# Optimization experiments

Hardware: AMD Instinct MI355X
Metric: run time of the kernel (lower is better)

Reference implementation:

```python
import jax, jax.numpy as jnp
import numpy as np

B, T, D, H = 1, 2048, 1024, 16
DH = D // H
DFF = 4 * D
SPARSITY_LAMBDA = 0.0005
LN_EPS = 1e-5


def _ln(x, g, b):
    mu = jnp.mean(x, axis=-1, keepdims=True)
    var = jnp.mean((x - mu) ** 2, axis=-1, keepdims=True)
    return (x - mu) * jax.lax.rsqrt(var + LN_EPS) * g + b


def setup_inputs() -> dict:
    key = jax.random.key(0)
    ks = jax.random.split(key, 8)
    s = lambda fan: 1.0 / np.sqrt(fan)
    inp = {
        "x": jax.random.normal(ks[0], (B, T, D), jnp.float32),
        "causal_mask": jnp.triu(jnp.ones((T, T), jnp.bool_), 1),
        "W_qkv": jax.random.normal(ks[1], (3 * D, D), jnp.float32) * s(D),
        "W_out": jax.random.normal(ks[2], (D, D), jnp.float32) * s(D),
        "log_mask": jnp.zeros((1, H, T, T), jnp.float32),
        "W_gate": jax.random.normal(ks[3], (D, 2 * D), jnp.float32) * s(2 * D),
        "b_gate": jnp.zeros((D,), jnp.float32),
        "g1": jnp.ones((D,), jnp.float32),
        "b1": jnp.zeros((D,), jnp.float32),
        "g2": jnp.ones((D,), jnp.float32),
        "b2": jnp.zeros((D,), jnp.float32),
        "W_ff1": jax.random.normal(ks[4], (DFF, D), jnp.float32) * s(D),
        "b_ff1": jnp.zeros((DFF,), jnp.float32),
        "W_ff2": jax.random.normal(ks[5], (D, DFF), jnp.float32) * s(DFF),
        "b_ff2": jnp.zeros((D,), jnp.float32),
    }
    return inp


def reference(x, causal_mask, W_qkv, W_out, log_mask, W_gate, b_gate,
              g1, b1, g2, b2, W_ff1, b_ff1, W_ff2, b_ff2):
    Bx, Tx, Dx = x.shape
    xn = _ln(x, g1, b1)
    qkv = xn @ W_qkv.T                              # [B,T,3D]
    q, k, v = jnp.split(qkv, 3, axis=-1)
    rs = lambda t: t.reshape(Bx, Tx, H, DH).transpose(0, 2, 1, 3)  # [B,H,T,dh]
    q, k, v = rs(q), rs(k), rs(v)
    scale = jnp.sqrt(jnp.asarray(DH, x.dtype))
    qk = jnp.einsum("bhtd,bhsd->bhts", q, k) / scale  # [B,H,T,T]
    cm = causal_mask[:Tx, :Tx]
    neg = jnp.asarray(-jnp.inf, x.dtype)
    # stream 1: plain causal softmax
    a_txt = jax.nn.softmax(jnp.where(cm, neg, qk), axis=-1)
    out_txt = jnp.einsum("bhts,bhsd->bhtd", a_txt, v)
    # stream 2: sigmoid-gated scores then causal softmax
    M = jax.nn.sigmoid(log_mask[:, :, :Tx, :Tx])
    a_cau = jax.nn.softmax(jnp.where(cm, neg, qk * M), axis=-1)
    out_cau = jnp.einsum("bhts,bhsd->bhtd", a_cau, v)
    merge = lambda t: t.transpose(0, 2, 1, 3).reshape(Bx, Tx, Dx)
    cat = jnp.concatenate([merge(out_txt), merge(out_cau)], axis=-1)  # [B,T,2D]
    a = (cat @ W_gate.T + b_gate) @ W_out.T
    sp = SPARSITY_LAMBDA * jnp.mean(M)
    # residual + FFN (dropout=0, eval mode)
    h = x + a
    hn = _ln(h, g2, b2)
    ff = jax.nn.gelu(hn @ W_ff1.T + b_ff1, approximate=False) @ W_ff2.T + b_ff2
    return h + ff, sp
```

## Files before the change

### kernel.cpp

```cpp
#include <hip/hip_runtime.h>
#include <hip/hip_bf16.h>

typedef __bf16 bf16x8 __attribute__((ext_vector_type(8)));
typedef _Float16 f16x4 __attribute__((ext_vector_type(4)));
typedef float f32x4 __attribute__((ext_vector_type(4)));

#define MFMA16(a, b, c) __builtin_amdgcn_mfma_f32_16x16x32_bf16(a, b, c, 0, 0, 0)
#define MFMA16H(a, b, c) __builtin_amdgcn_mfma_f32_16x16x16f16(a, b, c, 0, 0, 0)

#define T_SEQ 2048
#define D_MODEL 1024
#define N_HEADS 16
#define HEAD_DIM 64
#define D_FF 4096
#define QKV_STRIDE 3072

__device__ __forceinline__ float sigm(float x) { return 1.f / (1.f + __expf(-x)); }

__device__ __forceinline__ void g2l16(const void* g, void* l)
{
    __builtin_amdgcn_global_load_lds(
        (const __attribute__((address_space(1))) void*)g,
        (__attribute__((address_space(3))) void*)l, 16, 0, 0);
}

__device__ __forceinline__ float bperm(int srclane, float v)
{
    return __builtin_bit_cast(float,
        __builtin_amdgcn_ds_bpermute(srclane * 4, __builtin_bit_cast(int, v)));
}

#define N8_QKV 393216
#define N8_OUT 131072
#define N8_GATE 262144
#define N8_FF1 524288
#define N8_FF2 524288
__global__ __launch_bounds__(256) void cast_all_kernel(
    const float* __restrict__ s0, const float* __restrict__ s1,
    const float* __restrict__ s2, const float* __restrict__ s3,
    const float* __restrict__ s4,
    __bf16* __restrict__ d0, __bf16* __restrict__ d1, __bf16* __restrict__ d2,
    __bf16* __restrict__ d3, __bf16* __restrict__ d4, float* __restrict__ acc)
{
    int i = blockIdx.x * 256 + threadIdx.x;
    if (i == 0) acc[0] = 0.f;
    const float* s; __bf16* d; int j;
    if (i < N8_QKV)                           { s = s0; d = d0; j = i; }
    else if (i < N8_QKV + N8_OUT)             { s = s1; d = d1; j = i - N8_QKV; }
    else if (i < N8_QKV + N8_OUT + N8_GATE)   { s = s2; d = d2; j = i - N8_QKV - N8_OUT; }
    else if (i < N8_QKV + N8_OUT + N8_GATE + N8_FF1)
        { s = s3; d = d3; j = i - N8_QKV - N8_OUT - N8_GATE; }
    else { s = s4; d = d4; j = i - N8_QKV - N8_OUT - N8_GATE - N8_FF1; }
    const float4* p = (const float4*)s + (size_t)j * 2;
    float4 a = p[0], b = p[1];
    union { __bf16 h[8]; float4 v; } u;
    u.h[0] = (__bf16)a.x; u.h[1] = (__bf16)a.y; u.h[2] = (__bf16)a.z; u.h[3] = (__bf16)a.w;
    u.h[4] = (__bf16)b.x; u.h[5] = (__bf16)b.y; u.h[6] = (__bf16)b.z; u.h[7] = (__bf16)b.w;
    ((float4*)d)[j] = u.v;
}

__global__ __launch_bounds__(256) void ln_kernel(
    const float* __restrict__ x, const float* __restrict__ g,
    const float* __restrict__ b, __bf16* __restrict__ out)
{
    const int t = blockIdx.x;
    const int tid = threadIdx.x;
    float4 xv = *(const float4*)&x[t * D_MODEL + tid * 4];
    float s = xv.x + xv.y + xv.z + xv.w;
    float ss = xv.x * xv.x + xv.y * xv.y + xv.z * xv.z + xv.w * xv.w;
    for (int off = 1; off < 64; off <<= 1) {
        s += __shfl_xor(s, off);
        ss += __shfl_xor(ss, off);
    }
    __shared__ float sb[8];
    int w = tid >> 6, lane = tid & 63;
    if (lane == 0) { sb[w] = s; sb[4 + w] = ss; }
    __syncthreads();
    s = sb[0] + sb[1] + sb[2] + sb[3];
    ss = sb[4] + sb[5] + sb[6] + sb[7];
    float mu = s * (1.f / D_MODEL);
    float var = ss * (1.f / D_MODEL) - mu * mu;
    float rs = rsqrtf(var + 1e-5f);
    const float* xp = (const float*)&xv;
    for (int i = 0; i < 4; ++i) {
        int d = tid * 4 + i;
        out[t * D_MODEL + d] = (__bf16)((xp[i] - mu) * rs * g[d] + b[d]);
    }
}

template<int BM, int EPI>
__global__ __launch_bounds__(256) void gemm_nt(
    const __bf16* __restrict__ A, const __bf16* __restrict__ B,
    const float* __restrict__ bias,
    __bf16* __restrict__ outb, float* __restrict__ outf, _Float16* __restrict__ vtout,
    int M, int N, int klen, int lda)
{
    constexpr int BN = 128;
    constexpr int STAGE = (BM + BN) * 64 * 2;
    constexpr int CTB = (EPI == 3) ? BM * BN * 4 : (EPI == 4) ? BM * 132 * 4 : BM * BN * 2;
    constexpr int SMEM = (STAGE > CTB) ? STAGE : CTB;
    __shared__ __align__(16) char smem[SMEM];
    __bf16* As = (__bf16*)smem;
    __bf16* Bs = As + BM * 64;

    const int tid = threadIdx.x;
    const int lane = tid & 63, w = tid >> 6;
    const int quad = lane >> 4, l16 = lane & 15;
    const int bm = blockIdx.x * BM, bn = blockIdx.y * BN;
    const int koff = blockIdx.z * klen;
    if (EPI == 3) outf += (size_t)blockIdx.z * M * N;
    constexpr int NI = 4;
    constexpr int NJ = (BM == 128) ? 4 : 2;
    const int wm = (BM == 128) ? (w & 1) * 64 : 0;
    const int wn = (BM == 128) ? (w >> 1) * 64 : w * 32;

    f32x4 acc[NI][NJ] = {};

    for (int k0 = 0; k0 < klen; k0 += 64) {
        __syncthreads();
        constexpr int AIT = BM * 8 / 256;
        for (int it = 0; it < AIT; ++it) {
            int c = it * 256 + tid;
            int tile = (c >= BM * 4) ? 1 : 0;
            int c2 = c & (BM * 4 - 1);
            g2l16(&A[(size_t)(bm + (c2 >> 2)) * lda + koff + k0 + tile * 32 + ((c2 & 3) << 3)],
                  &As[c * 8]);
        }
        for (int it = 0; it < 4; ++it) {
            int c = it * 256 + tid;
            int tile = (c >= 512) ? 1 : 0;
            int c2 = c & 511;
            g2l16(&B[(size_t)(bn + (c2 >> 2)) * lda + koff + k0 + tile * 32 + ((c2 & 3) << 3)],
                  &Bs[c * 8]);
        }
        __syncthreads();
        for (int ks = 0; ks < 2; ++ks) {
            bf16x8 af[NI], bfr[NJ];
            for (int i = 0; i < NI; ++i)
                af[i] = *(const bf16x8*)&As[ks * BM * 32 + (wm + i * 16 + l16) * 32 + quad * 8];
            for (int j = 0; j < NJ; ++j)
                bfr[j] = *(const bf16x8*)&Bs[ks * BN * 32 + (wn + j * 16 + l16) * 32 + quad * 8];
            for (int i = 0; i < NI; ++i)
                for (int j = 0; j < NJ; ++j)
                    acc[i][j] = MFMA16(af[i], bfr[j], acc[i][j]);
        }
    }

    __syncthreads();
    if (EPI == 3) {
        float* Ct = (float*)smem;
        for (int i = 0; i < NI; ++i)
            for (int j = 0; j < NJ; ++j)
                for (int r = 0; r < 4; ++r)
                    Ct[(wm + i * 16 + quad * 4 + r) * BN + wn + j * 16 + l16] = acc[i][j][r];
        __syncthreads();
        constexpr int IT = BM * BN / 4 / 256;
        for (int it = 0; it < IT; ++it) {
            int c = it * 256 + tid;
            int row = c >> 5, col = (c & 31) << 2;
            *(float4*)&outf[(size_t)(bm + row) * N + bn + col] = *(float4*)&Ct[row * BN + col];
        }
    } else if (EPI == 4) {
        float* Ct = (float*)smem;
        for (int i = 0; i < NI; ++i)
            for (int j = 0; j < NJ; ++j)
                for (int r = 0; r < 4; ++r)
                    Ct[(wm + i * 16 + quad * 4 + r) * 132 + wn + j * 16 + l16] = acc[i][j][r];
        __syncthreads();
        if (bn < 2048) {
            for (int it = 0; it < BM * BN / 8 / 256; ++it) {
                int c = it * 256 + tid;
                int row = c >> 4, col8 = (c & 15) << 3;
                float4 f0 = *(float4*)&Ct[row * 132 + col8];
                float4 f1 = *(float4*)&Ct[row * 132 + col8 + 4];
                union { __bf16 h[8]; float4 v; } u;
                u.h[0] = (__bf16)f0.x; u.h[1] = (__bf16)f0.y; u.h[2] = (__bf16)f0.z; u.h[3] = (__bf16)f0.w;
                u.h[4] = (__bf16)f1.x; u.h[5] = (__bf16)f1.y; u.h[6] = (__bf16)f1.z; u.h[7] = (__bf16)f1.w;
                *(float4*)&outb[(size_t)(bm + row) * N + bn + col8] = u.v;
            }
        } else {
            int col = tid & 127;
            int r0 = (tid >> 7) * 32;
            int gcol = bn - 2048 + col;
            _Float16 buf[32];
            for (int r = 0; r < 32; ++r)
                buf[r] = (_Float16)Ct[(r0 + r) * 132 + col];
            _Float16* dst = &vtout[(size_t)gcol * T_SEQ + bm + r0];
            for (int k = 0; k < 4; ++k)
                *(float4*)&dst[k * 8] = *(float4*)&buf[k * 8];
        }
    } else {
        __bf16* Ct = (__bf16*)smem;
        for (int i = 0; i < NI; ++i)
            for (int j = 0; j < NJ; ++j)
                for (int r = 0; r < 4; ++r) {
                    int row = wm + i * 16 + quad * 4 + r;
                    int col = wn + j * 16 + l16;
                    float v = acc[i][j][r];
                    if (bias) v += bias[bn + col];
                    if (EPI == 1) v = 0.5f * v * (1.f + erff(v * 0.70710678118f));
                    Ct[row * BN + col] = (__bf16)v;
                }
        __syncthreads();
        constexpr int IT = BM * BN / 8 / 256;
        for (int it = 0; it < IT; ++it) {
            int c = it * 256 + tid;
            int row = c >> 4, col = (c & 15) << 3;
            *(float4*)&outb[(size_t)(bm + row) * N + bn + col] = *(float4*)&Ct[row * BN + col];
        }
    }
}

template<int MODE>
__global__ __launch_bounds__(256) void combine_kernel(
    const float* __restrict__ p0, const float* __restrict__ p1,
    const float* __restrict__ bias, const float* __restrict__ resid,
    __bf16* __restrict__ outb, float* __restrict__ outf,
    const float* __restrict__ sigacc)
{
    int i = blockIdx.x * 256 + threadIdx.x;
    float4 a = ((const float4*)p0)[i];
    float4 b = ((const float4*)p1)[i];
    int col = (i & 255) << 2;
    float4 bb = *(const float4*)&bias[col];
    float v[4] = {a.x + b.x + bb.x, a.y + b.y + bb.y, a.z + b.z + bb.z, a.w + b.w + bb.w};
    if (MODE == 2) {
        float4 r = ((const float4*)resid)[i];
        v[0] += r.x; v[1] += r.y; v[2] += r.z; v[3] += r.w;
        float4 o = {v[0], v[1], v[2], v[3]};
        ((float4*)outf)[i] = o;
        if (i == 0)
            outf[(size_t)T_SEQ * D_MODEL] = 0.0005f * sigacc[0] * (1.f / 67108864.f);
    } else {
        union { __bf16 h[4]; float2 f2; } u;
        for (int e = 0; e < 4; ++e) u.h[e] = (__bf16)v[e];
        ((float2*)outb)[i] = u.f2;
    }
}

__global__ __launch_bounds__(256) void combine_ln_kernel(
    const float* __restrict__ p0, const float* __restrict__ p1,
    const float* __restrict__ resid, const float* __restrict__ g,
    const float* __restrict__ b, float* __restrict__ h_out,
    __bf16* __restrict__ hn_out)
{
    const int t = blockIdx.x, tid = threadIdx.x;
    const int i = t * 256 + tid;
    float4 a = ((const float4*)p0)[i];
    float4 bb = ((const float4*)p1)[i];
    float4 r = ((const float4*)resid)[i];
    float4 v = {a.x + bb.x + r.x, a.y + bb.y + r.y, a.z + bb.z + r.z, a.w + bb.w + r.w};
    ((float4*)h_out)[i] = v;
    float s = v.x + v.y + v.z + v.w;
    float ss = v.x * v.x + v.y * v.y + v.z * v.z + v.w * v.w;
    for (int off = 1; off < 64; off <<= 1) {
        s += __shfl_xor(s, off);
        ss += __shfl_xor(ss, off);
    }
    __shared__ float sb[8];
    int w = tid >> 6, lane = tid & 63;
    if (lane == 0) { sb[w] = s; sb[4 + w] = ss; }
    __syncthreads();
    s = sb[0] + sb[1] + sb[2] + sb[3];
    ss = sb[4] + sb[5] + sb[6] + sb[7];
    float mu = s * (1.f / D_MODEL);
    float var = ss * (1.f / D_MODEL) - mu * mu;
    float rs = rsqrtf(var + 1e-5f);
    const float* vp = (const float*)&v;
    union { __bf16 h[4]; float2 f2; } u;
    for (int k = 0; k < 4; ++k) {
        int d = tid * 4 + k;
        u.h[k] = (__bf16)((vp[k] - mu) * rs * g[d] + b[d]);
    }
    ((float2*)hn_out)[i] = u.f2;
}

__global__ __launch_bounds__(256) void attn_split_kernel(
    const __bf16* __restrict__ qkv, const _Float16* __restrict__ vt,
    const float* __restrict__ lmask,
    __bf16* __restrict__ part_O, float2* __restrict__ part_ml,
    float* __restrict__ sigacc)
{
    __shared__ __bf16 KsAll[2 * 4096];
    __shared__ _Float16 VsAll[2 * 4096];

    const int tid = threadIdx.x;
    const int w = tid >> 6, lane = tid & 63;
    const int quad = lane >> 4, l16 = lane & 15;
    const int idx = blockIdx.x, h = blockIdx.y;
    int qt, sp;
    if (idx < 8)       { qt = idx;                sp = 0; }
    else if (idx < 24) { qt = 8 + ((idx - 8) >> 1);  sp = (idx - 8) & 1; }
    else if (idx < 48) { qt = 16 + (idx - 24) / 3;   sp = (idx - 24) % 3; }
    else               { qt = 24 + ((idx - 48) >> 2); sp = (idx - 48) & 3; }
    const int q0 = qt * 64;
    const int sbeg = sp * 512;
    const int send = min(sbeg + 512, q0 + 64);
    const int nch = (send - sbeg) >> 6;

    auto stage = [&](int s0, int bsel) {
        __bf16* kd = &KsAll[bsel * 4096];
        _Float16* vd = &VsAll[bsel * 4096];
        for (int it = 0; it < 2; ++it) {
            int c = it * 256 + tid;
            int tile = c >> 8, c2 = c & 255;
            g2l16(&qkv[(size_t)(s0 + (c2 >> 2)) * QKV_STRIDE + 1024 + h * 64 + tile * 32 + ((c2 & 3) << 3)],
                  &kd[c * 8]);
        }
        for (int it = 0; it < 2; ++it) {
            int c = it * 256 + tid;
            int dh = c >> 3, g = c & 7;
            int sIn = ((g + dh) & 7) * 8;
            g2l16(&vt[((size_t)h * 64 + dh) * T_SEQ + s0 + sIn], &vd[c * 8]);
        }
    };

    const int tq = q0 + w * 16 + l16;
    bf16x8 qf0 = *(const bf16x8*)&qkv[(size_t)tq * QKV_STRIDE + h * 64 + quad * 8];
    bf16x8 qf1 = *(const bf16x8*)&qkv[(size_t)tq * QKV_STRIDE + h * 64 + 32 + quad * 8];

    float m_[2] = {-1e30f, -1e30f}, l_[2] = {0.f, 0.f};
    f32x4 O[2][4] = {};
    float sigsum = 0.f;

    stage(sbeg, 0);

    for (int ci = 0; ci < nch; ++ci) {
        const int s0 = sbeg + (ci << 6);
        const int cur = ci & 1;
        __syncthreads();

        float4 lm[4];
        for (int c = 0; c < 4; ++c)
            lm[c] = *(const float4*)&lmask[((size_t)h * T_SEQ + tq) * T_SEQ + s0 + c * 16 + quad * 4];
        float4 up[4];
        const bool lower = (s0 + 64 <= q0);
        if (lower) {
            const float* upp = &lmask[((size_t)h * T_SEQ + s0 + (tid >> 2)) * T_SEQ + q0 + ((tid & 3) << 4)];
            for (int k = 0; k < 4; ++k) up[k] = *(const float4*)&upp[k * 4];
        }

        if (ci + 1 < nch) stage(s0 + 64, cur ^ 1);

        const __bf16* Ks = &KsAll[cur * 4096];
        const _Float16* Vs = &VsAll[cur * 4096];

        f32x4 St[4];
        for (int c = 0; c < 4; ++c) {
            bf16x8 kf0 = *(const bf16x8*)&Ks[(c * 16 + l16) * 32 + quad * 8];
            bf16x8 kf1 = *(const bf16x8*)&Ks[2048 + (c * 16 + l16) * 32 + quad * 8];
            f32x4 z = {};
            z = MFMA16(kf0, qf0, z);
            z = MFMA16(kf1, qf1, z);
            St[c] = z * 0.125f;
        }
        f16x4 vf[4][4];
        for (int c = 0; c < 4; ++c)
            for (int j = 0; j < 4; ++j) {
                int dh = j * 16 + l16;
                int gg = ((2 * c + (quad >> 1)) - dh) & 7;
                vf[c][j] = *(const f16x4*)&Vs[dh * 64 + gg * 8 + (quad & 1) * 4];
            }

        if (lower)
            for (int k = 0; k < 4; ++k) {
                const float* uu = (const float*)&up[k];
                sigsum += sigm(uu[0]) + sigm(uu[1]) + sigm(uu[2]) + sigm(uu[3]);
            }
        float sg[4][4];
        for (int c = 0; c < 4; ++c) {
            const float* lp = (const float*)&lm[c];
            for (int r = 0; r < 4; ++r) { sg[c][r] = sigm(lp[r]); sigsum += sg[c][r]; }
        }

        for (int v = 0; v < 2; ++v) {
            float p[4][4];
            float mx = -1e30f;
            for (int c = 0; c < 4; ++c) {
                int sbase = s0 + c * 16 + quad * 4;
                for (int r = 0; r < 4; ++r) {
                    float val = v ? St[c][r] * sg[c][r] : St[c][r];
                    val = (sbase + r > tq) ? -1e30f : val;
                    p[c][r] = val;
                    mx = fmaxf(mx, val);
                }
            }
            mx = fmaxf(mx, __shfl_xor(mx, 16));
            mx = fmaxf(mx, __shfl_xor(mx, 32));
            float mn = fmaxf(m_[v], mx);
            float al = __expf(m_[v] - mn);
            m_[v] = mn;
            float rs = 0.f;
            f16x4 pa[4];
            for (int c = 0; c < 4; ++c)
                for (int r = 0; r < 4; ++r) {
                    float e = __expf(p[c][r] - mn);
                    rs += e;
                    pa[c][r] = (_Float16)e;
                }
            rs += __shfl_xor(rs, 16);
            rs += __shfl_xor(rs, 32);
            l_[v] = l_[v] * al + rs;
            float alO[4];
            for (int r = 0; r < 4; ++r) alO[r] = bperm(quad * 4 + r, al);
            for (int j = 0; j < 4; ++j)
                for (int r = 0; r < 4; ++r) O[v][j][r] *= alO[r];
            for (int c = 0; c < 4; ++c)
                for (int j = 0; j < 4; ++j)
                    O[v][j] = MFMA16H(pa[c], vf[c][j], O[v][j]);
        }
    }

    const size_t slot = (size_t)h * 80 + idx;
    for (int v = 0; v < 2; ++v)
        for (int j = 0; j < 4; ++j)
            for (int r = 0; r < 4; ++r) {
                int row = w * 16 + quad * 4 + r;
                part_O[((slot * 2 + v) * 64 + row) * 64 + j * 16 + l16] = (__bf16)O[v][j][r];
            }
    if (quad == 0)
        for (int v = 0; v < 2; ++v)
            part_ml[(slot * 2 + v) * 64 + w * 16 + l16] = make_float2(m_[v], l_[v]);
    for (int off = 1; off < 64; off <<= 1) sigsum += __shfl_xor(sigsum, off);
    if (lane == 0) atomicAdd(sigacc, sigsum);
}

__global__ __launch_bounds__(256) void attn_combine_kernel(
    const __bf16* __restrict__ part_O, const float2* __restrict__ part_ml,
    __bf16* __restrict__ cat)
{
    const int qt = blockIdx.x, h = blockIdx.y;
    const int nsp = (qt >> 3) + 1;
    const int base = (qt < 8) ? qt : (qt < 16) ? 8 + (qt - 8) * 2
                   : (qt < 24) ? 24 + (qt - 16) * 3 : 48 + (qt - 24) * 4;
    const int tid = threadIdx.x;
    const int row = tid >> 2, v = (tid >> 1) & 1, colh = (tid & 1) * 32;

    float2 ml[4];
    float M = -1e30f;
    for (int p = 0; p < nsp; ++p) {
        ml[p] = part_ml[(((size_t)h * 80 + base + p) * 2 + v) * 64 + row];
        M = fmaxf(M, ml[p].x);
    }
    float L = 0.f;
    float acc[32] = {};
    for (int p = 0; p < nsp; ++p) {
        float sc = __expf(ml[p].x - M);
        L += sc * ml[p].y;
        const __bf16* src =
            &part_O[((((size_t)h * 80 + base + p) * 2 + v) * 64 + row) * 64 + colh];
        for (int k = 0; k < 4; ++k) {
            bf16x8 o = *(const bf16x8*)&src[k * 8];
            for (int e = 0; e < 8; ++e) acc[k * 8 + e] += sc * (float)o[e];
        }
    }
    float inv = 1.f / L;
    __bf16* dst = &cat[(size_t)(qt * 64 + row) * 2048 + v * 1024 + h * 64 + colh];
    for (int k = 0; k < 4; ++k) {
        union { __bf16 hh[8]; float4 f4; } u;
        for (int e = 0; e < 8; ++e) u.hh[e] = (__bf16)(acc[k * 8 + e] * inv);
        *(float4*)&dst[k * 8] = u.f4;
    }
}

extern "C" void kernel_launch(void* const* d_in, const int* in_sizes, int n_in,
                              void* d_out, int out_size, void* d_ws, size_t ws_size,
                              hipStream_t stream)
{
    const float* x      = (const float*)d_in[0];
    const float* W_qkv  = (const float*)d_in[2];
    const float* W_out  = (const float*)d_in[3];
    const float* lmask  = (const float*)d_in[4];
    const float* W_gate = (const float*)d_in[5];
    const float* b_gate = (const float*)d_in[6];
    const float* g1     = (const float*)d_in[7];
    const float* b1     = (const float*)d_in[8];
    const float* g2     = (const float*)d_in[9];
    const float* b2     = (const float*)d_in[10];
    const float* W_ff1  = (const float*)d_in[11];
    const float* b_ff1  = (const float*)d_in[12];
    const float* W_ff2  = (const float*)d_in[13];
    const float* b_ff2  = (const float*)d_in[14];
    float* out = (float*)d_out;

    char* ws = (char*)d_ws;
    size_t off = 0;
    auto alloc = [&](size_t bytes) {
        char* p = ws + off;
        off += (bytes + 255) & ~(size_t)255;
        return p;
    };
    __bf16* wq_b   = (__bf16*)alloc((size_t)3072 * 1024 * 2);
    __bf16* wout_b = (__bf16*)alloc((size_t)1024 * 1024 * 2);
    __bf16* wg_b   = (__bf16*)alloc((size_t)1024 * 2048 * 2);
    __bf16* wf1_b  = (__bf16*)alloc((size_t)4096 * 1024 * 2);
    __bf16* wf2_b  = (__bf16*)alloc((size_t)1024 * 4096 * 2);
    __bf16* xn_b   = (__bf16*)alloc((size_t)2048 * 1024 * 2);
    __bf16* qkv_b  = (__bf16*)alloc((size_t)2048 * 3072 * 2);
    _Float16* vt_h = (_Float16*)alloc((size_t)16 * 64 * 2048 * 2);
    __bf16* cat_b  = (__bf16*)alloc((size_t)2048 * 2048 * 2);
    __bf16* a1_b   = (__bf16*)alloc((size_t)2048 * 1024 * 2);
    float*  h_f    = (float*)alloc((size_t)2048 * 1024 * 4);
    __bf16* hn_b   = (__bf16*)alloc((size_t)2048 * 1024 * 2);
    __bf16* e_b    = (__bf16*)alloc((size_t)2048 * 4096 * 2);
    __bf16* part_O = (__bf16*)alloc((size_t)16 * 80 * 2 * 64 * 64 * 2);
    float2* part_ml= (float2*)alloc((size_t)16 * 80 * 2 * 64 * 8);
    float*  psum   = (float*)alloc((size_t)2 * 2048 * 1024 * 4);
    float*  acc    = (float*)alloc(256);
    float*  psum1  = psum + (size_t)2048 * 1024;

    cast_all_kernel<<<7168, 256, 0, stream>>>(W_qkv, W_out, W_gate, W_ff1, W_ff2,
                                              wq_b, wout_b, wg_b, wf1_b, wf2_b, acc);
    ln_kernel<<<2048, 256, 0, stream>>>(x, g1, b1, xn_b);
    gemm_nt<64, 4><<<dim3(32, 24), 256, 0, stream>>>(xn_b, wq_b, nullptr, qkv_b, nullptr, vt_h, 2048, 3072, 1024, 1024);
    attn_split_kernel<<<dim3(80, 16), 256, 0, stream>>>(qkv_b, vt_h, lmask, part_O, part_ml, acc);
    attn_combine_kernel<<<dim3(32, 16), 256, 0, stream>>>(part_O, part_ml, cat_b);
    gemm_nt<64, 3><<<dim3(32, 8, 2), 256, 0, stream>>>(cat_b, wg_b, nullptr, nullptr, psum, nullptr, 2048, 1024, 1024, 2048);
    combine_kernel<0><<<2048, 256, 0, stream>>>(psum, psum1, b_gate, nullptr, a1_b, nullptr, nullptr);
    gemm_nt<64, 3><<<dim3(32, 8, 2), 256, 0, stream>>>(a1_b, wout_b, nullptr, nullptr, psum, nullptr, 2048, 1024, 512, 1024);
    combine_ln_kernel<<<2048, 256, 0, stream>>>(psum, psum1, x, g2, b2, h_f, hn_b);
    gemm_nt<128, 1><<<dim3(16, 32), 256, 0, stream>>>(hn_b, wf1_b, b_ff1, e_b, nullptr, nullptr, 2048, 4096, 1024, 1024);
    gemm_nt<64, 3><<<dim3(32, 8, 2), 256, 0, stream>>>(e_b, wf2_b, nullptr, nullptr, psum, nullptr, 2048, 1024, 2048, 4096);
    combine_kernel<2><<<2048, 256, 0, stream>>>(psum, psum1, b_ff2, h_f, nullptr, out, acc);

    (void)in_sizes; (void)n_in; (void)out_size; (void)ws_size;
}
```

Baseline: 667.6 us.

## Double-buffer GEMM LDS tiles and prefetch log_mask one chunk ahead in attention

The GEMM kernel now uses two LDS stages: the next K tile is issued with global_load_lds while the current tile is consumed, which drops one barrier per iteration. The attention kernel loads the next chunk's log_mask row and transposed tiles into registers before computing the current chunk, so global latency hides behind the MFMA and softmax work. In exchange, GEMM LDS use doubles, which may lower occupancy, and the register prefetch raises VGPR pressure.

```diff
diff --git a/kernel.cpp b/kernel.cpp
--- a/kernel.cpp
+++ b/kernel.cpp
@@ -96,12 +96,11 @@
     int M, int N, int klen, int lda)
 {
     constexpr int BN = 128;
-    constexpr int STAGE = (BM + BN) * 64 * 2;
+    constexpr int SBUF = (BM + BN) * 64 * 2;
+    constexpr int STAGE = SBUF * 2;
     constexpr int CTB = (EPI == 3) ? BM * BN * 4 : (EPI == 4) ? BM * 132 * 4 : BM * BN * 2;
     constexpr int SMEM = (STAGE > CTB) ? STAGE : CTB;
     __shared__ __align__(16) char smem[SMEM];
-    __bf16* As = (__bf16*)smem;
-    __bf16* Bs = As + BM * 64;
 
     const int tid = threadIdx.x;
     const int lane = tid & 63, w = tid >> 6;
@@ -114,10 +113,9 @@
     const int wm = (BM == 128) ? (w & 1) * 64 : 0;
     const int wn = (BM == 128) ? (w >> 1) * 64 : w * 32;
 
-    f32x4 acc[NI][NJ] = {};
-
-    for (int k0 = 0; k0 < klen; k0 += 64) {
-        __syncthreads();
+    auto stageg = [&](int k0, int b) {
+        __bf16* As = (__bf16*)(smem + b * SBUF);
+        __bf16* Bs = As + BM * 64;
         constexpr int AIT = BM * 8 / 256;
         for (int it = 0; it < AIT; ++it) {
             int c = it * 256 + tid;
@@ -133,7 +131,17 @@
             g2l16(&B[(size_t)(bn + (c2 >> 2)) * lda + koff + k0 + tile * 32 + ((c2 & 3) << 3)],
                   &Bs[c * 8]);
         }
+    };
+
+    f32x4 acc[NI][NJ] = {};
+    const int nkt = klen >> 6;
+    stageg(0, 0);
+
+    for (int kt = 0; kt < nkt; ++kt) {
         __syncthreads();
+        if (kt + 1 < nkt) stageg((kt + 1) << 6, (kt + 1) & 1);
+        const __bf16* As = (const __bf16*)(smem + (kt & 1) * SBUF);
+        const __bf16* Bs = As + BM * 64;
         for (int ks = 0; ks < 2; ++ks) {
             bf16x8 af[NI], bfr[NJ];
             for (int i = 0; i < NI; ++i)
@@ -298,6 +306,8 @@
     const int send = min(sbeg + 512, q0 + 64);
     const int nch = (send - sbeg) >> 6;
 
+    const int tq = q0 + w * 16 + l16;
+
     auto stage = [&](int s0, int bsel) {
         __bf16* kd = &KsAll[bsel * 4096];
         _Float16* vd = &VsAll[bsel * 4096];
@@ -314,8 +324,15 @@
             g2l16(&vt[((size_t)h * 64 + dh) * T_SEQ + s0 + sIn], &vd[c * 8]);
         }
     };
-
-    const int tq = q0 + w * 16 + l16;
+    auto load_lm = [&](int s0, float4* dst) {
+        for (int c = 0; c < 4; ++c)
+            dst[c] = *(const float4*)&lmask[((size_t)h * T_SEQ + tq) * T_SEQ + s0 + c * 16 + quad * 4];
+    };
+    auto load_up = [&](int s0, float4* dst) {
+        const float* upp = &lmask[((size_t)h * T_SEQ + s0 + (tid >> 2)) * T_SEQ + q0 + ((tid & 3) << 4)];
+        for (int k = 0; k < 4; ++k) dst[k] = *(const float4*)&upp[k * 4];
+    };
+
     bf16x8 qf0 = *(const bf16x8*)&qkv[(size_t)tq * QKV_STRIDE + h * 64 + quad * 8];
     bf16x8 qf1 = *(const bf16x8*)&qkv[(size_t)tq * QKV_STRIDE + h * 64 + 32 + quad * 8];
 
@@ -323,24 +340,19 @@
     f32x4 O[2][4] = {};
     float sigsum = 0.f;
 
+    float4 lmc[4], upc[4], lmn[4], upn[4];
     stage(sbeg, 0);
+    load_lm(sbeg, lmc);
+    bool lower_c = (sbeg + 64 <= q0);
+    if (lower_c) load_up(sbeg, upc);
 
     for (int ci = 0; ci < nch; ++ci) {
         const int s0 = sbeg + (ci << 6);
         const int cur = ci & 1;
         __syncthreads();
 
-        float4 lm[4];
-        for (int c = 0; c < 4; ++c)
-            lm[c] = *(const float4*)&lmask[((size_t)h * T_SEQ + tq) * T_SEQ + s0 + c * 16 + quad * 4];
-        float4 up[4];
-        const bool lower = (s0 + 64 <= q0);
-        if (lower) {
-            const float* upp = &lmask[((size_t)h * T_SEQ + s0 + (tid >> 2)) * T_SEQ + q0 + ((tid & 3) << 4)];
-            for (int k = 0; k < 4; ++k) up[k] = *(const float4*)&upp[k * 4];
-        }
-
-        if (ci + 1 < nch) stage(s0 + 64, cur ^ 1);
+        const bool has_next = (ci + 1 < nch);
+        if (has_next) stage(s0 + 64, cur ^ 1);
 
         const __bf16* Ks = &KsAll[cur * 4096];
         const _Float16* Vs = &VsAll[cur * 4096];
@@ -362,14 +374,21 @@
                 vf[c][j] = *(const f16x4*)&Vs[dh * 64 + gg * 8 + (quad & 1) * 4];
             }
 
-        if (lower)
+        bool lower_n = false;
+        if (has_next) {
+            load_lm(s0 + 64, lmn);
+            lower_n = (s0 + 128 <= q0);
+            if (lower_n) load_up(s0 + 64, upn);
+        }
+
+        if (lower_c)
             for (int k = 0; k < 4; ++k) {
-                const float* uu = (const float*)&up[k];
+                const float* uu = (const float*)&upc[k];
                 sigsum += sigm(uu[0]) + sigm(uu[1]) + sigm(uu[2]) + sigm(uu[3]);
             }
         float sg[4][4];
         for (int c = 0; c < 4; ++c) {
-            const float* lp = (const float*)&lm[c];
+            const float* lp = (const float*)&lmc[c];
             for (int r = 0; r < 4; ++r) { sg[c][r] = sigm(lp[r]); sigsum += sg[c][r]; }
         }
 
@@ -409,6 +428,10 @@
                 for (int j = 0; j < 4; ++j)
                     O[v][j] = MFMA16H(pa[c], vf[c][j], O[v][j]);
         }
+
+        for (int c = 0; c < 4; ++c) lmc[c] = lmn[c];
+        if (lower_n) for (int k = 0; k < 4; ++k) upc[k] = upn[k];
+        lower_c = lower_n;
     }
 
     const size_t slot = (size_t)h * 80 + idx;
```

Result: no change. 656.3 us (-1.7%).
